# Optimization experiments

Measured on AMD Instinct MI355X. Metric: run time of the kernel, lower is better.

The kernel has to match this reference:

```python
import jax, jax.numpy as jnp
import numpy as np

_SAMPLING_EPS = 1e-5


def setup_inputs() -> dict:
    key = jax.random.key(0)
    k1, k2, k3, k4, k5 = jax.random.split(key, 5)
    B, V = 128, 128000
    logits = jax.random.normal(k1, (B, V), dtype=jnp.float32)
    temperature = jax.random.uniform(k2, (B,), dtype=jnp.float32, minval=0.0, maxval=1.5)
    top_p = jax.random.uniform(k3, (B,), dtype=jnp.float32, minval=0.1, maxval=1.0)
    top_k = jax.random.randint(k4, (B,), 1, 64, dtype=jnp.int32)
    u = jax.random.uniform(k5, (B, V), dtype=jnp.float32, minval=1e-9, maxval=1.0)
    gumbel = -jnp.log(-jnp.log(u))  # standard Gumbel noise for the sampling trick
    return {"logits": logits, "temperature": temperature, "top_p": top_p,
            "top_k": top_k, "gumbel": gumbel, "num_logprobs": 20}


def reference(logits, temperature, top_p, top_k, gumbel, num_logprobs):
    logits = logits.astype(jnp.float32)
    B, V = logits.shape
    # step 1: raw logprobs (logprobs_mode == 'raw_logprobs')
    raw_logprobs = jax.nn.log_softmax(logits, axis=-1)
    # greedy sample (before temperature, which is argmax-invariant anyway)
    greedy = jnp.argmax(logits, axis=-1)
    # apply temperature (greedy rows get temp=1 to avoid div-by-0)
    temp_safe = jnp.where(temperature < _SAMPLING_EPS, 1.0, temperature)
    scaled = logits / temp_safe[:, None]
    # sort descending once; do top-k and top-p masking in sorted space
    sorted_idx = jnp.argsort(-scaled, axis=-1)                     # [B,V] int
    sorted_logits = jnp.take_along_axis(scaled, sorted_idx, axis=-1)
    k = jnp.clip(top_k, 1, V)
    keep_k = jnp.arange(V, dtype=jnp.int32)[None, :] < k[:, None]
    probs_sorted = jax.nn.softmax(sorted_logits, axis=-1)
    cum = jnp.cumsum(probs_sorted, axis=-1)
    # keep smallest prefix with cumulative prob >= top_p (token 0 always kept)
    keep_p = (cum - probs_sorted) <= top_p[:, None]
    masked_sorted = jnp.where(keep_k & keep_p, sorted_logits, -jnp.inf)
    # multinomial sampling via Gumbel-max in sorted space, map back to vocab ids
    gumbel_sorted = jnp.take_along_axis(gumbel, sorted_idx, axis=-1)
    pos = jnp.argmax(masked_sorted + gumbel_sorted, axis=-1)
    random_sampled = jnp.take_along_axis(sorted_idx, pos[:, None], axis=-1)[:, 0]
    sampled = jnp.where(temperature < _SAMPLING_EPS, greedy, random_sampled)
    # gather_logprobs: top-k logprobs + sampled token logprob + rank
    topk_logprobs, topk_indices = jax.lax.top_k(raw_logprobs, num_logprobs)
    token_logprobs = jnp.take_along_axis(raw_logprobs, sampled[:, None], axis=-1)  # [B,1]
    token_ranks = (jnp.sum(raw_logprobs > token_logprobs, axis=-1) + 1).astype(jnp.int32)
    indices = jnp.concatenate([sampled[:, None], topk_indices], axis=1).astype(jnp.int32)
    logprobs_out = jnp.concatenate([token_logprobs, topk_logprobs], axis=1)
    sampled_token_ids = sampled.astype(jnp.int32)[:, None]  # [B,1]
    return sampled_token_ids, indices, logprobs_out, token_ranks
```

## Files before the change

### kernel.cpp

```cpp
#include <hip/hip_runtime.h>
#include <math.h>

#define SAMPLING_EPS 1e-5f
#define TCAND 2.8f
#define SPLITS 16
#define BLOCK_A 256
#define BLOCK_B 256
#define CAPL 2048
#define NBIN 4096

__device__ __forceinline__ unsigned f2u(float f) {
  unsigned b = __float_as_uint(f);
  return (b & 0x80000000u) ? ~b : (b | 0x80000000u);
}

__device__ __forceinline__ void redCombine(float& m, int& mi, float& sr, float& ss,
                                           float om, int omi, float osr, float oss,
                                           float its) {
  float nm = fmaxf(m, om);
  float e1 = (m == nm) ? 1.0f : expf(m - nm);
  float e2 = (om == nm) ? 1.0f : expf(om - nm);
  float f1 = (m == nm) ? 1.0f : expf((m - nm) * its);
  float f2 = (om == nm) ? 1.0f : expf((om - nm) * its);
  sr = sr * e1 + osr * e2;
  ss = ss * f1 + oss * f2;
  if (om > m || (om == m && omi < mi)) mi = omi;
  m = nm;
}

__device__ __forceinline__ void procElem(float x, int gidx,
                                         float& m, int& mi, float& sr, float& ss,
                                         float its, unsigned* crow,
                                         float* cvrow, int* cirow, int cap) {
  if (x > m) {
    float d = m - x;
    sr = sr * expf(d) + 1.0f;
    ss = ss * expf(d * its) + 1.0f;
    m = x; mi = gidx;
  } else {
    float d = x - m;
    sr += expf(d);
    ss += expf(d * its);
  }
  if (x > TCAND) {
    unsigned p = atomicAdd(crow, 1u);
    if (p < (unsigned)cap) { cvrow[p] = x; cirow[p] = gidx; }
  }
}

__global__ void __launch_bounds__(BLOCK_A) sampler_pass1(
    const float* __restrict__ logits, const float* __restrict__ temperature,
    float4* __restrict__ partials, unsigned* __restrict__ cnt,
    float* __restrict__ candV, int* __restrict__ candI,
    int V, int cap) {
  const int row = blockIdx.y;
  const int chunk = blockIdx.x;
  const int S = gridDim.x;
  const int tid = threadIdx.x;
  const int CH = ((V + S - 1) / S + 3) & ~3;
  const int start = chunk * CH;
  const int end = (start + CH < V) ? (start + CH) : V;

  if (start >= end) {
    if (tid == 0) partials[row * S + chunk] = make_float4(-INFINITY, __int_as_float(0), 0.f, 0.f);
    return;
  }

  float temp = temperature[row];
  float ts = (temp < SAMPLING_EPS) ? 1.0f : temp;
  float its = 1.0f / ts;

  const float* lr = logits + (size_t)row * V;
  unsigned* crow = cnt + row;
  float* cvrow = candV + (size_t)row * cap;
  int* cirow = candI + (size_t)row * cap;

  float m = -INFINITY; int mi = 0; float sr = 0.f, ss = 0.f;

  const int n = end - start;
  const int n4 = n >> 2;
  const float4* p4 = reinterpret_cast<const float4*>(lr + start);
  for (int j = tid; j < n4; j += BLOCK_A) {
    float4 x4 = p4[j];
    int gbase = start + (j << 2);
    procElem(x4.x, gbase + 0, m, mi, sr, ss, its, crow, cvrow, cirow, cap);
    procElem(x4.y, gbase + 1, m, mi, sr, ss, its, crow, cvrow, cirow, cap);
    procElem(x4.z, gbase + 2, m, mi, sr, ss, its, crow, cvrow, cirow, cap);
    procElem(x4.w, gbase + 3, m, mi, sr, ss, its, crow, cvrow, cirow, cap);
  }
  for (int i = start + (n4 << 2) + tid; i < end; i += BLOCK_A) {
    procElem(lr[i], i, m, mi, sr, ss, its, crow, cvrow, cirow, cap);
  }

  for (int off = 32; off > 0; off >>= 1) {
    float om = __shfl_down(m, off);
    int omi = __shfl_down(mi, off);
    float osr = __shfl_down(sr, off);
    float oss = __shfl_down(ss, off);
    redCombine(m, mi, sr, ss, om, omi, osr, oss, its);
  }
  __shared__ float wm[BLOCK_A / 64], wsr[BLOCK_A / 64], wss[BLOCK_A / 64];
  __shared__ int wmi[BLOCK_A / 64];
  int wave = tid >> 6, lane = tid & 63;
  if (lane == 0) { wm[wave] = m; wmi[wave] = mi; wsr[wave] = sr; wss[wave] = ss; }
  __syncthreads();
  if (tid == 0) {
    for (int w = 1; w < BLOCK_A / 64; ++w)
      redCombine(m, mi, sr, ss, wm[w], wmi[w], wsr[w], wss[w], its);
    partials[row * S + chunk] = make_float4(m, __int_as_float(mi), sr, ss);
  }
}

__global__ void __launch_bounds__(BLOCK_B) sampler_finalize(
    const float* __restrict__ logits, const float* __restrict__ temperature,
    const float* __restrict__ top_p, const int* __restrict__ top_k,
    const float* __restrict__ gumbel,
    const float4* __restrict__ partials, const unsigned* __restrict__ cnt,
    const float* __restrict__ candV, const int* __restrict__ candI,
    float* __restrict__ out_ids, float* __restrict__ out_idx,
    float* __restrict__ out_lp, float* __restrict__ out_rank,
    int V, int S, int L, int cap, int NTOP) {
  const int row = blockIdx.x;
  const int tid = threadIdx.x;

  __shared__ float sV[CAPL];
  __shared__ int   sI[CAPL];
  __shared__ float sLp[CAPL];
  __shared__ float sSc[CAPL];
  __shared__ int   hist[NBIN];
  __shared__ float posSc[128], posLp[128];
  __shared__ int   posIdx[128];
  __shared__ float topLp[128];
  __shared__ int   topIdx[128];
  __shared__ float gscore[128], pexp[128];
  __shared__ float shM, shSr, shSs, shLpSel;
  __shared__ int   shGi;
  __shared__ unsigned uEdge;
  __shared__ int   fcnt;
  __shared__ int   wred[BLOCK_B / 64];

  float temp = temperature[row];
  float ts = (temp < SAMPLING_EPS) ? 1.0f : temp;

  if (tid == 0) {
    float m = -INFINITY; int mi = 0; float sr = 0.f, ss = 0.f;
    float its = 1.0f / ts;
    for (int s = 0; s < S; ++s) {
      float4 p = partials[row * S + s];
      redCombine(m, mi, sr, ss, p.x, __float_as_int(p.y), p.z, p.w, its);
    }
    shM = m; shGi = mi; shSr = sr; shSs = ss;
  }
  __syncthreads();
  const float M = shM;
  const float Ss = shSs;
  const float logSr = logf(shSr);

  unsigned c = (cap > 0) ? cnt[row] : 0u;
  int C;
  if (cap > 0 && c >= (unsigned)NTOP && c <= (unsigned)cap) {
    C = (int)c;
    for (int i = tid; i < C; i += BLOCK_B) {
      float v = candV[(size_t)row * cap + i];
      int id = candI[(size_t)row * cap + i];
      sV[i] = v; sI[i] = id;
      sLp[i] = (v - M) - logSr;
      sSc[i] = v / ts;
    }
    __syncthreads();
  } else {
    const float* lr = logits + (size_t)row * V;
    for (int i = tid; i < NBIN; i += BLOCK_B) hist[i] = 0;
    __syncthreads();
    for (int i = tid; i < V; i += BLOCK_B) atomicAdd(&hist[f2u(lr[i]) >> 20], 1);
    __syncthreads();
    if (tid == 0) {
      int acc = 0, eb = 0;
      for (int b = NBIN - 1; b >= 0; --b) { acc += hist[b]; if (acc >= NTOP) { eb = b; break; } }
      uEdge = ((unsigned)eb) << 20;
      fcnt = 0;
    }
    __syncthreads();
    for (int i = tid; i < V; i += BLOCK_B) {
      float x = lr[i];
      if (f2u(x) >= uEdge) {
        int p = atomicAdd(&fcnt, 1);
        if (p < CAPL) { sV[p] = x; sI[p] = i; }
      }
    }
    __syncthreads();
    C = (fcnt < CAPL) ? fcnt : CAPL;
    for (int i = tid; i < C; i += BLOCK_B) {
      float v = sV[i];
      sLp[i] = (v - M) - logSr;
      sSc[i] = v / ts;
    }
    __syncthreads();
  }

  const int NT = (C < NTOP) ? C : NTOP;

  for (int i = tid; i < C; i += BLOCK_B) {
    float sci = sSc[i], lpi = sLp[i];
    int ii = sI[i];
    int rA = 0, rB = 0;
    for (int j = 0; j < C; ++j) {
      float scj = sSc[j], lpj = sLp[j];
      int ij = sI[j];
      rA += (scj > sci) || (scj == sci && ij < ii);
      rB += (lpj > lpi) || (lpj == lpi && ij < ii);
    }
    if (rA < NT) { posSc[rA] = sci; posLp[rA] = lpi; posIdx[rA] = ii; }
    if (rB < NT) { topLp[rB] = lpi; topIdx[rB] = ii; }
  }
  __syncthreads();

  const float Msc = M / ts;
  if (tid < NT) {
    float sc = posSc[tid];
    gscore[tid] = sc + gumbel[(size_t)row * V + posIdx[tid]];
    pexp[tid] = expf(sc - Msc) / Ss;
  }
  __syncthreads();

  if (tid == 0) {
    int k = top_k[row];
    if (k < 1) k = 1;
    if (k > V) k = V;
    float tp = top_p[row];
    float cum = 0.f, best = -INFINITY;
    int bpos = 0;
    for (int j = 0; j < NT; ++j) {
      float p = pexp[j];
      cum += p;
      if (j < k && (cum - p) <= tp) {
        float s = gscore[j];
        if (s > best) { best = s; bpos = j; }
      }
    }
    int sampled; float lpsel;
    if (temp < SAMPLING_EPS) {
      sampled = shGi;
      lpsel = 0.0f - logSr;
    } else {
      sampled = posIdx[bpos];
      lpsel = posLp[bpos];
    }
    shLpSel = lpsel;
    out_ids[row] = (float)sampled;
    out_idx[row * (L + 1)] = (float)sampled;
    out_lp[row * (L + 1)] = lpsel;
  }
  __syncthreads();

  float lpsel = shLpSel;
  int cg = 0;
  for (int i = tid; i < C; i += BLOCK_B) cg += (sLp[i] > lpsel) ? 1 : 0;
  for (int off = 32; off > 0; off >>= 1) cg += __shfl_down(cg, off);
  if ((tid & 63) == 0) wred[tid >> 6] = cg;
  __syncthreads();
  if (tid == 0) {
    int t = 0;
    for (int w = 0; w < BLOCK_B / 64; ++w) t += wred[w];
    out_rank[row] = (float)(t + 1);
  }

  if (tid < L && tid < NT) {
    out_idx[row * (L + 1) + 1 + tid] = (float)topIdx[tid];
    out_lp[row * (L + 1) + 1 + tid] = topLp[tid];
  }
}

extern "C" void kernel_launch(void* const* d_in, const int* in_sizes, int n_in,
                              void* d_out, int out_size, void* d_ws, size_t ws_size,
                              hipStream_t stream) {
  const float* logits      = (const float*)d_in[0];
  const float* temperature = (const float*)d_in[1];
  const float* top_p       = (const float*)d_in[2];
  const int*   top_k       = (const int*)d_in[3];
  const float* gumbel      = (const float*)d_in[4];

  const int B = in_sizes[1];
  const int V = in_sizes[0] / B;
  int L = out_size / (2 * B) - 2;
  if (L < 0) L = 0;
  int NTOP = 64;
  if (L > 64) NTOP = (L <= 128) ? L : 128;

  int S = SPLITS;
  unsigned char* ws = (unsigned char*)d_ws;
  size_t cntBytes = ((size_t)B * 4 + 255) & ~(size_t)255;
  while (S > 1 && cntBytes + (size_t)B * S * sizeof(float4) > ws_size) S >>= 1;
  unsigned* cnt = (unsigned*)ws;
  float4* partials = (float4*)(ws + cntBytes);
  size_t off = cntBytes + (size_t)B * S * sizeof(float4);
  off = (off + 255) & ~(size_t)255;
  size_t rem = (ws_size > off) ? (ws_size - off) : 0;
  int cap = (int)(rem / ((size_t)B * 8));
  if (cap > 1024) cap = 1024;
  if (cap < 0) cap = 0;
  float* candV = (float*)(ws + off);
  int*   candI = (int*)(ws + off + (size_t)B * cap * 4);

  hipMemsetAsync(cnt, 0, (size_t)B * 4, stream);

  dim3 gA(S, B);
  sampler_pass1<<<gA, BLOCK_A, 0, stream>>>(logits, temperature, partials, cnt,
                                            candV, candI, V, cap);

  float* out_f = (float*)d_out;
  float* out_ids = out_f;
  float* out_idx = out_f + B;
  float* out_lp = out_f + B + B * (L + 1);
  float* out_rank = out_f + B + 2 * B * (L + 1);

  sampler_finalize<<<B, BLOCK_B, 0, stream>>>(logits, temperature, top_p, top_k, gumbel,
                                              partials, cnt, candV, candI,
                                              out_ids, out_idx, out_lp, out_rank,
                                              V, S, L, cap, NTOP);
}
```

Measured before the change: 262.3 us.

## Restructure pass1 into register-tiled blocks with two-pass local softmax

Pass 1 stops using 16 large splits per row with a per-element online softmax. Each block now loads a fixed 5 float4 per thread into registers, takes the local max, then sums the exponentials in a second pass over the registers with fast __expf. The grid grows to about 25 chunks per row. Argmax tracking is dropped, and the greedy token is taken from the top-k candidate list instead. This removes the per-element rescaling exps and branches and exposes more memory-level parallelism. In exchange it writes more partials, removes the workspace-size fallback for S, and the greedy path now depends on the candidate list being valid.

Result: slower. 333.5 us (+27.1%).

```diff
diff --git a/kernel.cpp b/kernel.cpp
--- a/kernel.cpp
+++ b/kernel.cpp
@@ -3,8 +3,8 @@
 
 #define SAMPLING_EPS 1e-5f
 #define TCAND 2.8f
-#define SPLITS 16
 #define BLOCK_A 256
+#define KF4 5
 #define BLOCK_B 256
 #define CAPL 2048
 #define NBIN 4096
@@ -14,38 +14,17 @@
   return (b & 0x80000000u) ? ~b : (b | 0x80000000u);
 }
 
-__device__ __forceinline__ void redCombine(float& m, int& mi, float& sr, float& ss,
-                                           float om, int omi, float osr, float oss,
+__device__ __forceinline__ void redCombine(float& m, float& sr, float& ss,
+                                           float om, float osr, float oss,
                                            float its) {
   float nm = fmaxf(m, om);
-  float e1 = (m == nm) ? 1.0f : expf(m - nm);
-  float e2 = (om == nm) ? 1.0f : expf(om - nm);
-  float f1 = (m == nm) ? 1.0f : expf((m - nm) * its);
-  float f2 = (om == nm) ? 1.0f : expf((om - nm) * its);
+  float e1 = (m == nm) ? 1.0f : __expf(m - nm);
+  float e2 = (om == nm) ? 1.0f : __expf(om - nm);
+  float f1 = (m == nm) ? 1.0f : __expf((m - nm) * its);
+  float f2 = (om == nm) ? 1.0f : __expf((om - nm) * its);
   sr = sr * e1 + osr * e2;
   ss = ss * f1 + oss * f2;
-  if (om > m || (om == m && omi < mi)) mi = omi;
   m = nm;
-}
-
-__device__ __forceinline__ void procElem(float x, int gidx,
-                                         float& m, int& mi, float& sr, float& ss,
-                                         float its, unsigned* crow,
-                                         float* cvrow, int* cirow, int cap) {
-  if (x > m) {
-    float d = m - x;
-    sr = sr * expf(d) + 1.0f;
-    ss = ss * expf(d * its) + 1.0f;
-    m = x; mi = gidx;
-  } else {
-    float d = x - m;
-    sr += expf(d);
-    ss += expf(d * its);
-  }
-  if (x > TCAND) {
-    unsigned p = atomicAdd(crow, 1u);
-    if (p < (unsigned)cap) { cvrow[p] = x; cirow[p] = gidx; }
-  }
 }
 
 __global__ void __launch_bounds__(BLOCK_A) sampler_pass1(
@@ -57,57 +36,93 @@
   const int chunk = blockIdx.x;
   const int S = gridDim.x;
   const int tid = threadIdx.x;
-  const int CH = ((V + S - 1) / S + 3) & ~3;
-  const int start = chunk * CH;
-  const int end = (start + CH < V) ? (start + CH) : V;
-
-  if (start >= end) {
-    if (tid == 0) partials[row * S + chunk] = make_float4(-INFINITY, __int_as_float(0), 0.f, 0.f);
-    return;
-  }
+  const int f4row = V >> 2;
+  const int base = chunk * (BLOCK_A * KF4);
+  const float* lr = logits + (size_t)row * V;
+  const float4* p4 = reinterpret_cast<const float4*>(lr);
 
   float temp = temperature[row];
   float ts = (temp < SAMPLING_EPS) ? 1.0f : temp;
   float its = 1.0f / ts;
 
-  const float* lr = logits + (size_t)row * V;
-  unsigned* crow = cnt + row;
-  float* cvrow = candV + (size_t)row * cap;
-  int* cirow = candI + (size_t)row * cap;
-
-  float m = -INFINITY; int mi = 0; float sr = 0.f, ss = 0.f;
-
-  const int n = end - start;
-  const int n4 = n >> 2;
-  const float4* p4 = reinterpret_cast<const float4*>(lr + start);
-  for (int j = tid; j < n4; j += BLOCK_A) {
-    float4 x4 = p4[j];
-    int gbase = start + (j << 2);
-    procElem(x4.x, gbase + 0, m, mi, sr, ss, its, crow, cvrow, cirow, cap);
-    procElem(x4.y, gbase + 1, m, mi, sr, ss, its, crow, cvrow, cirow, cap);
-    procElem(x4.z, gbase + 2, m, mi, sr, ss, its, crow, cvrow, cirow, cap);
-    procElem(x4.w, gbase + 3, m, mi, sr, ss, its, crow, cvrow, cirow, cap);
-  }
-  for (int i = start + (n4 << 2) + tid; i < end; i += BLOCK_A) {
-    procElem(lr[i], i, m, mi, sr, ss, its, crow, cvrow, cirow, cap);
-  }
-
+  float x[KF4 * 4];
+  int gj[KF4];
+  #pragma unroll
+  for (int k = 0; k < KF4; ++k) {
+    int j = base + tid + k * BLOCK_A;
+    gj[k] = j;
+    if (j < f4row) {
+      float4 v = p4[j];
+      x[4 * k + 0] = v.x; x[4 * k + 1] = v.y;
+      x[4 * k + 2] = v.z; x[4 * k + 3] = v.w;
+    } else {
+      x[4 * k + 0] = -INFINITY; x[4 * k + 1] = -INFINITY;
+      x[4 * k + 2] = -INFINITY; x[4 * k + 3] = -INFINITY;
+    }
+  }
+
+  float m = -INFINITY;
+  #pragma unroll
+  for (int e = 0; e < KF4 * 4; ++e) m = fmaxf(m, x[e]);
+  float mc = fmaxf(m, -1.0e37f);
+
+  float sr0 = 0.f, sr1 = 0.f, ss0 = 0.f, ss1 = 0.f;
+  #pragma unroll
+  for (int e = 0; e < KF4 * 4; e += 2) {
+    float d0 = x[e] - mc, d1 = x[e + 1] - mc;
+    sr0 += __expf(d0);
+    sr1 += __expf(d1);
+    ss0 += __expf(d0 * its);
+    ss1 += __expf(d1 * its);
+  }
+  float sr = sr0 + sr1, ss = ss0 + ss1;
+
+  #pragma unroll
+  for (int k = 0; k < KF4; ++k) {
+    #pragma unroll
+    for (int e = 0; e < 4; ++e) {
+      float xv = x[4 * k + e];
+      if (xv > TCAND) {
+        unsigned p = atomicAdd(cnt + row, 1u);
+        if (p < (unsigned)cap) {
+          candV[(size_t)row * cap + p] = xv;
+          candI[(size_t)row * cap + p] = (gj[k] << 2) + e;
+        }
+      }
+    }
+  }
+
+  if ((V & 3) && chunk == 0 && tid == 0) {
+    for (int i = (f4row << 2); i < V; ++i) {
+      float xv = lr[i];
+      redCombine(mc, sr, ss, xv, 1.0f, 1.0f, its);
+      m = fmaxf(m, xv);
+      if (xv > TCAND) {
+        unsigned p = atomicAdd(cnt + row, 1u);
+        if (p < (unsigned)cap) {
+          candV[(size_t)row * cap + p] = xv;
+          candI[(size_t)row * cap + p] = i;
+        }
+      }
+    }
+  }
+
+  float mm = (m == -INFINITY) ? -INFINITY : mc;
+  #pragma unroll
   for (int off = 32; off > 0; off >>= 1) {
-    float om = __shfl_down(m, off);
-    int omi = __shfl_down(mi, off);
+    float om = __shfl_down(mm, off);
     float osr = __shfl_down(sr, off);
     float oss = __shfl_down(ss, off);
-    redCombine(m, mi, sr, ss, om, omi, osr, oss, its);
+    redCombine(mm, sr, ss, om, osr, oss, its);
   }
   __shared__ float wm[BLOCK_A / 64], wsr[BLOCK_A / 64], wss[BLOCK_A / 64];
-  __shared__ int wmi[BLOCK_A / 64];
   int wave = tid >> 6, lane = tid & 63;
-  if (lane == 0) { wm[wave] = m; wmi[wave] = mi; wsr[wave] = sr; wss[wave] = ss; }
+  if (lane == 0) { wm[wave] = mm; wsr[wave] = sr; wss[wave] = ss; }
   __syncthreads();
   if (tid == 0) {
     for (int w = 1; w < BLOCK_A / 64; ++w)
-      redCombine(m, mi, sr, ss, wm[w], wmi[w], wsr[w], wss[w], its);
-    partials[row * S + chunk] = make_float4(m, __int_as_float(mi), sr, ss);
+      redCombine(mm, sr, ss, wm[w], wsr[w], wss[w], its);
+    partials[row * S + chunk] = make_float4(mm, 0.f, sr, ss);
   }
 }
 
@@ -134,7 +149,6 @@
   __shared__ int   topIdx[128];
   __shared__ float gscore[128], pexp[128];
   __shared__ float shM, shSr, shSs, shLpSel;
-  __shared__ int   shGi;
   __shared__ unsigned uEdge;
   __shared__ int   fcnt;
   __shared__ int   wred[BLOCK_B / 64];
@@ -143,13 +157,13 @@
   float ts = (temp < SAMPLING_EPS) ? 1.0f : temp;
 
   if (tid == 0) {
-    float m = -INFINITY; int mi = 0; float sr = 0.f, ss = 0.f;
+    float m = -INFINITY, sr = 0.f, ss = 0.f;
     float its = 1.0f / ts;
     for (int s = 0; s < S; ++s) {
       float4 p = partials[row * S + s];
-      redCombine(m, mi, sr, ss, p.x, __float_as_int(p.y), p.z, p.w, its);
-    }
-    shM = m; shGi = mi; shSr = sr; shSs = ss;
+      redCombine(m, sr, ss, p.x, p.z, p.w, its);
+    }
+    shM = m; shSr = sr; shSs = ss;
   }
   __syncthreads();
   const float M = shM;
@@ -240,8 +254,8 @@
     }
     int sampled; float lpsel;
     if (temp < SAMPLING_EPS) {
-      sampled = shGi;
-      lpsel = 0.0f - logSr;
+      sampled = topIdx[0];
+      lpsel = topLp[0];
     } else {
       sampled = posIdx[bpos];
       lpsel = posLp[bpos];
@@ -287,10 +301,12 @@
   int NTOP = 64;
   if (L > 64) NTOP = (L <= 128) ? L : 128;
 
-  int S = SPLITS;
+  const int f4row = V >> 2;
+  int S = (f4row + BLOCK_A * KF4 - 1) / (BLOCK_A * KF4);
+  if (S < 1) S = 1;
+
   unsigned char* ws = (unsigned char*)d_ws;
   size_t cntBytes = ((size_t)B * 4 + 255) & ~(size_t)255;
-  while (S > 1 && cntBytes + (size_t)B * S * sizeof(float4) > ws_size) S >>= 1;
   unsigned* cnt = (unsigned*)ws;
   float4* partials = (float4*)(ws + cntBytes);
   size_t off = cntBytes + (size_t)B * S * sizeof(float4);
```
